# Performance work log

Hardware: AMD Instinct MI355X
Metric: run time of the kernel (lower is better)

## Reference

```python
import jax, jax.numpy as jnp
import numpy as np

PH, PW = 7, 7          # pooled output size
SR = 2                 # sampling_ratio (fixed grid per bin)
SCALE = 0.0625         # spatial_scale = 1/16


def _axis(v, size):
    """Per-axis bilinear setup, faithful to the original clamping logic.
    v: [K] float sample coords. Returns lo, hi int indices, frac l, 1-l, valid mask."""
    valid = (v >= -1.0) & (v <= size)
    vc = jnp.maximum(v, 0.0)
    lo0 = jnp.floor(vc).astype(jnp.int32)
    at_edge = lo0 >= size - 1
    lo = jnp.where(at_edge, size - 1, lo0)
    hi = jnp.where(at_edge, size - 1, lo0 + 1)
    vc = jnp.where(at_edge, jnp.asarray(size - 1, vc.dtype), vc)
    l = vc - lo.astype(vc.dtype)
    return lo, hi, l, 1.0 - l, valid


def roi_align(feat, rois):
    B, C, H, W = feat.shape
    feat_flat = feat.reshape(B, C, H * W)
    grid = (jnp.arange(SR, dtype=feat.dtype) + 0.5) / SR  # sub-bin offsets

    def per_roi(roi):
        b = roi[0].astype(jnp.int32)
        sw, sh = roi[1] * SCALE, roi[2] * SCALE
        ew, eh = roi[3] * SCALE, roi[4] * SCALE
        rw = jnp.maximum(ew - sw, 1.0)
        rh = jnp.maximum(eh - sh, 1.0)
        bh, bw = rh / PH, rw / PW
        # sample coordinates: y[PH,SR], x[PW,SR]
        y = sh + jnp.arange(PH, dtype=feat.dtype)[:, None] * bh + grid[None, :] * bh
        x = sw + jnp.arange(PW, dtype=feat.dtype)[:, None] * bw + grid[None, :] * bw
        y_lo, y_hi, ly, hy, vy = _axis(y.reshape(-1), H)  # [PH*SR]
        x_lo, x_hi, lx, hx, vx = _axis(x.reshape(-1), W)  # [PW*SR]
        valid = (vy[:, None] & vx[None, :]).astype(feat.dtype)  # out-of-range -> zero contribution
        w1 = hy[:, None] * hx[None, :] * valid
        w2 = hy[:, None] * lx[None, :] * valid
        w3 = ly[:, None] * hx[None, :] * valid
        w4 = ly[:, None] * lx[None, :] * valid
        i1 = y_lo[:, None] * W + x_lo[None, :]
        i2 = y_lo[:, None] * W + x_hi[None, :]
        i3 = y_hi[:, None] * W + x_lo[None, :]
        i4 = y_hi[:, None] * W + x_hi[None, :]
        fb = jnp.take(feat_flat, b, axis=0)  # [C, H*W]
        # gather + weighted sum -> [C, PH*SR, PW*SR]
        s = (jnp.take(fb, i1, axis=1) * w1 + jnp.take(fb, i2, axis=1) * w2
             + jnp.take(fb, i3, axis=1) * w3 + jnp.take(fb, i4, axis=1) * w4)
        # average over the SR x SR sampling grid per bin (== / count)
        return s.reshape(C, PH, SR, PW, SR).mean(axis=(2, 4))  # [C, PH, PW]

    return jax.vmap(per_roi)(rois)  # [N, C, PH, PW]


def setup_inputs() -> dict:
    key = jax.random.key(0)
    k1, k2, k3, k4, k5 = jax.random.split(key, 5)
    bottom_data = jax.random.normal(k1, (1, 1024, 50, 50), dtype=jnp.float32)
    n_rois, img = 512, 800.0
    x1 = jax.random.uniform(k2, (n_rois,), minval=0.0, maxval=img - 64.0)
    y1 = jax.random.uniform(k3, (n_rois,), minval=0.0, maxval=img - 64.0)
    bw = jax.random.uniform(k4, (n_rois,), minval=32.0, maxval=256.0)
    bh = jax.random.uniform(k5, (n_rois,), minval=32.0, maxval=256.0)
    x2 = jnp.minimum(x1 + bw, img)
    y2 = jnp.minimum(y1 + bh, img)
    bottom_rois = jnp.stack([jnp.zeros((n_rois,)), x1, y1, x2, y2], axis=1).astype(jnp.float32)
    return {"bottom_data": bottom_data, "bottom_rois": bottom_rois}


def reference(bottom_data, bottom_rois):
    return roi_align(bottom_data, bottom_rois)
```

## Files before the change

kernel.cpp:

```cpp
#include <hip/hip_runtime.h>

#define PH 7
#define PW 7
#define SCALE 0.0625f
#define C_TOTAL 1024
#define H_ 50
#define W_ 50
#define HW_TOTAL (H_ * W_)
#define NROIS 512
#define NBIN (PH * PW)
#define CHB 64
#define NCHUNK (C_TOTAL / CHB)
#define ROWB (W_ * C_TOTAL * 4)
#define COLB (C_TOTAL * 4)
#define RMAX 17
#define GP   65

__global__ __launch_bounds__(256) void transpose_kernel(
    const float* __restrict__ feat, float* __restrict__ featT)
{
    __shared__ float tile[64][65];
    const int hw0 = (blockIdx.x % 40) * 64;
    const int c0  = (blockIdx.x / 40) * 64;
    const int tx = threadIdx.x & 63;
    const int ty = threadIdx.x >> 6;

    const int hw_r = hw0 + tx;
    if (hw_r < HW_TOTAL) {
        #pragma unroll
        for (int j = 0; j < 16; ++j) {
            const int c_l = j * 4 + ty;
            tile[c_l][tx] = feat[(size_t)(c0 + c_l) * HW_TOTAL + hw_r];
        }
    }
    __syncthreads();
    #pragma unroll
    for (int j = 0; j < 16; ++j) {
        const int hw_l = j * 4 + ty;
        const int hw = hw0 + hw_l;
        if (hw < HW_TOTAL)
            featT[(size_t)hw * C_TOTAL + c0 + tx] = tile[tx][hw_l];
    }
}

__device__ __forceinline__ float ldf(const char* base, unsigned byte_off) {
    return *reinterpret_cast<const float*>(base + byte_off);
}

__device__ __forceinline__ float rfl_f(float v) {
    return __uint_as_float(__builtin_amdgcn_readfirstlane(__float_as_uint(v)));
}

__global__ __launch_bounds__(512, 6) void roi_sep_kernel(
    const float* __restrict__ featT,
    const float* __restrict__ rois,
    float* __restrict__ out)
{
    __shared__ __align__(16) float s_G[RMAX * 7 * GP];
    __shared__ __align__(16) int   s_xoff[7][4];
    __shared__ __align__(16) float s_xw[7][4];
    __shared__ __align__(16) int   s_yiT[4][NBIN];
    __shared__ __align__(16) float s_ywT[4][NBIN];

    const int blk    = blockIdx.x;
    const int roi_id = blk >> 4;
    const int chunk  = blk & (NCHUNK - 1);
    const int tid    = threadIdx.x;

    const float* roi = rois + roi_id * 5;

    const float shy = roi[2] * SCALE, ehy = roi[4] * SCALE;
    const float rht = fmaxf(ehy - shy, 1.0f);
    const float bh  = rht * (1.0f / 7.0f);
    int r0 = (int)floorf(fmaxf(shy + 0.25f * bh, 0.0f));
    if (r0 > H_ - 1) r0 = H_ - 1;
    const int lol = (int)floorf(fmaxf(shy + 6.75f * bh, 0.0f));
    int r1 = (lol >= H_ - 1) ? (H_ - 1) : (lol + 1);
    if (r1 - r0 + 1 > RMAX) r1 = r0 + RMAX - 1;
    const int R  = r1 - r0 + 1;

    if (tid < 7) {
        const float swx = roi[1] * SCALE, ewx = roi[3] * SCALE;
        const float rwd = fmaxf(ewx - swx, 1.0f);
        const float bw  = rwd * (1.0f / 7.0f);
        const float base = swx + (float)tid * bw;
        const float v0 = base + 0.25f * bw;
        const float v1 = base + 0.75f * bw;

        int lo0, hi0, lo1, hi1;
        float l0, h0, l1, h1, m0, m1;
        {
            const bool val = (v0 >= -1.0f) && (v0 <= (float)W_);
            float vc = fmaxf(v0, 0.0f);
            int lo = (int)floorf(vc);
            if (lo >= W_ - 1) { lo0 = W_ - 1; hi0 = W_ - 1; vc = (float)(W_ - 1); }
            else              { lo0 = lo; hi0 = lo + 1; }
            l0 = vc - (float)lo0; h0 = 1.0f - l0;
            m0 = val ? 1.0f : 0.0f;
        }
        {
            const bool val = (v1 >= -1.0f) && (v1 <= (float)W_);
            float vc = fmaxf(v1, 0.0f);
            int lo = (int)floorf(vc);
            if (lo >= W_ - 1) { lo1 = W_ - 1; hi1 = W_ - 1; vc = (float)(W_ - 1); }
            else              { lo1 = lo; hi1 = lo + 1; }
            l1 = vc - (float)lo1; h1 = 1.0f - l1;
            m1 = val ? 1.0f : 0.0f;
        }

        float W0 = h0 * m0, W1 = l0 * m0, W2 = h1 * m1, W3 = l1 * m1;
        int I0 = lo0, I1 = hi0, I2 = lo1, I3 = hi1;
        if (I1 == I0) { W0 += W1; W1 = 0.0f; }
        if (I2 == I0) { W0 += W2; W2 = 0.0f; }
        else if (I2 == I1) { W1 += W2; W2 = 0.0f; }
        if (I3 == I0) { W0 += W3; W3 = 0.0f; }
        else if (I3 == I1) { W1 += W3; W3 = 0.0f; }
        else if (I3 == I2) { W2 += W3; W3 = 0.0f; }

        #define CSH(A, B) if (W##A == 0.0f && W##B != 0.0f) { W##A = W##B; I##A = I##B; W##B = 0.0f; }
        CSH(0,1) CSH(1,2) CSH(2,3)
        CSH(0,1) CSH(1,2) CSH(2,3)
        CSH(0,1) CSH(1,2) CSH(2,3)
        #undef CSH

        s_xoff[tid][0] = I0 * COLB; s_xoff[tid][1] = I1 * COLB;
        s_xoff[tid][2] = I2 * COLB; s_xoff[tid][3] = I3 * COLB;
        s_xw[tid][0] = W0; s_xw[tid][1] = W1; s_xw[tid][2] = W2; s_xw[tid][3] = W3;
    }

    if (tid >= 64 && tid < 64 + NBIN) {
        const int bin = tid - 64;
        const int py  = bin / 7, px = bin - py * 7;
        const float base = shy + (float)py * bh;
        const float v0 = base + 0.25f * bh;
        const float v1 = base + 0.75f * bh;

        int lo0, hi0, lo1, hi1;
        float l0, h0, l1, h1, m0, m1;
        {
            const bool val = (v0 >= -1.0f) && (v0 <= (float)H_);
            float vc = fmaxf(v0, 0.0f);
            int lo = (int)floorf(vc);
            if (lo >= H_ - 1) { lo0 = H_ - 1; hi0 = H_ - 1; vc = (float)(H_ - 1); }
            else              { lo0 = lo; hi0 = lo + 1; }
            l0 = vc - (float)lo0; h0 = 1.0f - l0;
            m0 = val ? 0.25f : 0.0f;
        }
        {
            const bool val = (v1 >= -1.0f) && (v1 <= (float)H_);
            float vc = fmaxf(v1, 0.0f);
            int lo = (int)floorf(vc);
            if (lo >= H_ - 1) { lo1 = H_ - 1; hi1 = H_ - 1; vc = (float)(H_ - 1); }
            else              { lo1 = lo; hi1 = lo + 1; }
            l1 = vc - (float)lo1; h1 = 1.0f - l1;
            m1 = val ? 0.25f : 0.0f;
        }

        const int s0 = min(lo0 - r0, RMAX - 1), s1 = min(hi0 - r0, RMAX - 1);
        const int s2 = min(lo1 - r0, RMAX - 1), s3 = min(hi1 - r0, RMAX - 1);
        s_yiT[0][bin] = (s0 * 7 + px) * GP;
        s_yiT[1][bin] = (s1 * 7 + px) * GP;
        s_yiT[2][bin] = (s2 * 7 + px) * GP;
        s_yiT[3][bin] = (s3 * 7 + px) * GP;
        s_ywT[0][bin] = h0 * m0; s_ywT[1][bin] = l0 * m0;
        s_ywT[2][bin] = h1 * m1; s_ywT[3][bin] = l1 * m1;
    }
    __syncthreads();

    int   xo_s[7][4];
    float xw_s[7][4];
    #pragma unroll
    for (int i = 0; i < 7; ++i) {
        const int4   t = *(const int4*)  s_xoff[i];
        const float4 w = *(const float4*)s_xw[i];
        xo_s[i][0] = __builtin_amdgcn_readfirstlane(t.x);
        xo_s[i][1] = __builtin_amdgcn_readfirstlane(t.y);
        xo_s[i][2] = __builtin_amdgcn_readfirstlane(t.z);
        xo_s[i][3] = __builtin_amdgcn_readfirstlane(t.w);
        xw_s[i][0] = rfl_f(w.x); xw_s[i][1] = rfl_f(w.y);
        xw_s[i][2] = rfl_f(w.z); xw_s[i][3] = rfl_f(w.w);
    }

    const int wave = tid >> 6, lane = tid & 63;
    const char* fb  = (const char*)featT;
    const int laneB = (chunk * CHB + lane) * 4;

    for (int rs = wave; rs < R; rs += 8) {
        const unsigned rb = (unsigned)(laneB + (r0 + rs) * ROWB);
        float f[7][4];
        #pragma unroll
        for (int px = 0; px < 7; ++px) {
            f[px][0] = ldf(fb + xo_s[px][0], rb);
            f[px][1] = ldf(fb + xo_s[px][1], rb);
            f[px][2] = ldf(fb + xo_s[px][2], rb);
            f[px][3] = ldf(fb + xo_s[px][3], rb);
        }
        __asm__ __volatile__("" ::: "memory");
        float* gbase = &s_G[rs * 7 * GP + lane];
        #pragma unroll
        for (int px = 0; px < 7; ++px) {
            gbase[px * GP] = (xw_s[px][0] * f[px][0] + xw_s[px][1] * f[px][1])
                           + (xw_s[px][2] * f[px][2] + xw_s[px][3] * f[px][3]);
        }
    }
    __syncthreads();

    float* obase = out + (size_t)roi_id * (C_TOTAL * NBIN)
                       + (size_t)chunk * CHB * NBIN;
    #pragma unroll
    for (int q = 0; q < 3; ++q) {
        const int o   = tid + (q << 9);
        const int c   = o / NBIN;
        const int bin = o - c * NBIN;
        const int i0 = s_yiT[0][bin], i1 = s_yiT[1][bin];
        const int i2 = s_yiT[2][bin], i3 = s_yiT[3][bin];
        const float w0 = s_ywT[0][bin], w1 = s_ywT[1][bin];
        const float w2 = s_ywT[2][bin], w3 = s_ywT[3][bin];
        const float a0 = (w0 * s_G[i0 + c]      + w1 * s_G[i1 + c])
                       + (w2 * s_G[i2 + c]      + w3 * s_G[i3 + c]);
        const float a1 = (w0 * s_G[i0 + c + 32] + w1 * s_G[i1 + c + 32])
                       + (w2 * s_G[i2 + c + 32] + w3 * s_G[i3 + c + 32]);
        __builtin_nontemporal_store(a0, obase + o);
        __builtin_nontemporal_store(a1, obase + o + 1568);
    }
    if (tid < 32) {
        const int o   = tid + 1536;
        const int c   = 31;
        const int bin = o - c * NBIN;
        const int i0 = s_yiT[0][bin], i1 = s_yiT[1][bin];
        const int i2 = s_yiT[2][bin], i3 = s_yiT[3][bin];
        const float w0 = s_ywT[0][bin], w1 = s_ywT[1][bin];
        const float w2 = s_ywT[2][bin], w3 = s_ywT[3][bin];
        const float a0 = (w0 * s_G[i0 + c]      + w1 * s_G[i1 + c])
                       + (w2 * s_G[i2 + c]      + w3 * s_G[i3 + c]);
        const float a1 = (w0 * s_G[i0 + c + 32] + w1 * s_G[i1 + c + 32])
                       + (w2 * s_G[i2 + c + 32] + w3 * s_G[i3 + c + 32]);
        __builtin_nontemporal_store(a0, obase + o);
        __builtin_nontemporal_store(a1, obase + o + 1568);
    }
}

__global__ __launch_bounds__(256) void roi_align_fallback(
    const float* __restrict__ feat,
    const float* __restrict__ rois,
    float* __restrict__ out)
{
    __shared__ float s_w[16][NBIN];
    __shared__ int   s_i[16][NBIN];

    const int blk    = blockIdx.x;
    const int roi_id = blk >> 3;
    const int chunk  = blk & 7;
    const int tid    = threadIdx.x;

    const float* roi = rois + roi_id * 5;

    if (tid < NBIN * 4) {
        const float swx = roi[1] * SCALE;
        const float shy = roi[2] * SCALE;
        const float ewx = roi[3] * SCALE;
        const float ehy = roi[4] * SCALE;
        const float rw = fmaxf(ewx - swx, 1.0f);
        const float rh = fmaxf(ehy - shy, 1.0f);
        const float bw = rw * (1.0f / PW);
        const float bh = rh * (1.0f / PH);

        const int bin = tid >> 2;
        const int s   = tid & 3;
        const int iy  = s >> 1, ix = s & 1;
        const int py  = bin / PW, px = bin % PW;

        const float y = shy + ((float)py + ((float)iy + 0.5f) * 0.5f) * bh;
        const float x = swx + ((float)px + ((float)ix + 0.5f) * 0.5f) * bw;

        const bool vy = (y >= -1.0f) && (y <= (float)H_);
        float yc = fmaxf(y, 0.0f);
        int ylo = (int)floorf(yc);
        int yhi;
        if (ylo >= H_ - 1) { ylo = H_ - 1; yhi = H_ - 1; yc = (float)(H_ - 1); }
        else               { yhi = ylo + 1; }
        const float ly = yc - (float)ylo;
        const float hy = 1.0f - ly;

        const bool vx = (x >= -1.0f) && (x <= (float)W_);
        float xc = fmaxf(x, 0.0f);
        int xlo = (int)floorf(xc);
        int xhi;
        if (xlo >= W_ - 1) { xlo = W_ - 1; xhi = W_ - 1; xc = (float)(W_ - 1); }
        else               { xhi = xlo + 1; }
        const float lx = xc - (float)xlo;
        const float hx = 1.0f - lx;

        const float v = (vy && vx) ? 0.25f : 0.0f;

        const int r = s * 4;
        s_w[r + 0][bin] = hy * hx * v;
        s_w[r + 1][bin] = hy * lx * v;
        s_w[r + 2][bin] = ly * hx * v;
        s_w[r + 3][bin] = ly * lx * v;
        s_i[r + 0][bin] = ylo * W_ + xlo;
        s_i[r + 1][bin] = ylo * W_ + xhi;
        s_i[r + 2][bin] = yhi * W_ + xlo;
        s_i[r + 3][bin] = yhi * W_ + xhi;
    }
    __syncthreads();

    const float* fbase = feat + (size_t)chunk * 128 * HW_TOTAL;
    float* obase = out + (size_t)roi_id * (C_TOTAL * NBIN)
                       + (size_t)chunk * 128 * NBIN;

    for (int o = tid; o < 128 * NBIN; o += 256) {
        const int c   = o / NBIN;
        const int bin = o - c * NBIN;
        const float* f = fbase + c * HW_TOTAL;
        float acc = 0.0f;
        #pragma unroll
        for (int r = 0; r < 16; ++r) acc += s_w[r][bin] * f[s_i[r][bin]];
        obase[o] = acc;
    }
}

extern "C" void kernel_launch(void* const* d_in, const int* in_sizes, int n_in,
                              void* d_out, int out_size, void* d_ws, size_t ws_size,
                              hipStream_t stream) {
    const float* feat = (const float*)d_in[0];
    const float* rois = (const float*)d_in[1];
    float* out = (float*)d_out;

    const size_t need = (size_t)HW_TOTAL * C_TOTAL * sizeof(float);
    if (ws_size >= need) {
        float* featT = (float*)d_ws;
        transpose_kernel<<<dim3(40 * (C_TOTAL / 64)), dim3(256), 0, stream>>>(feat, featT);
        roi_sep_kernel<<<dim3(NROIS * NCHUNK), dim3(512), 0, stream>>>(featT, rois, out);
    } else {
        roi_align_fallback<<<dim3(NROIS * 8), dim3(256), 0, stream>>>(feat, rois, out);
    }
}
```

Before: 54.62 us.

## Precompute per-ROI bilinear tables in the transpose kernel and load them in ROI kernel

The per-ROI x and y sample offsets, weights, r0 and R are now computed once per ROI by the first 512 blocks of the transpose kernel and written to a table after featT in the workspace. The ROI kernel loads these tables from global memory instead of recomputing them in each of its 16 channel-chunk blocks. This removes the redundant setup math and the setup barrier before the gather phase. In exchange it adds global loads of the table, slightly more workspace, and extra work in the transpose kernel.

```diff
diff --git a/kernel.cpp b/kernel.cpp
--- a/kernel.cpp
+++ b/kernel.cpp
@@ -16,8 +16,12 @@
 #define RMAX 17
 #define GP   65
 
+#define TBL_OFF    (HW_TOTAL * C_TOTAL)
+#define TBL_STRIDE 512
+
 __global__ __launch_bounds__(256) void transpose_kernel(
-    const float* __restrict__ feat, float* __restrict__ featT)
+    const float* __restrict__ feat, float* __restrict__ featT,
+    const float* __restrict__ rois)
 {
     __shared__ float tile[64][65];
     const int hw0 = (blockIdx.x % 40) * 64;
@@ -41,33 +45,13 @@
         if (hw < HW_TOTAL)
             featT[(size_t)hw * C_TOTAL + c0 + tx] = tile[tx][hw_l];
     }
-}
-
-__device__ __forceinline__ float ldf(const char* base, unsigned byte_off) {
-    return *reinterpret_cast<const float*>(base + byte_off);
-}
-
-__device__ __forceinline__ float rfl_f(float v) {
-    return __uint_as_float(__builtin_amdgcn_readfirstlane(__float_as_uint(v)));
-}
-
-__global__ __launch_bounds__(512, 6) void roi_sep_kernel(
-    const float* __restrict__ featT,
-    const float* __restrict__ rois,
-    float* __restrict__ out)
-{
-    __shared__ __align__(16) float s_G[RMAX * 7 * GP];
-    __shared__ __align__(16) int   s_xoff[7][4];
-    __shared__ __align__(16) float s_xw[7][4];
-    __shared__ __align__(16) int   s_yiT[4][NBIN];
-    __shared__ __align__(16) float s_ywT[4][NBIN];
-
-    const int blk    = blockIdx.x;
-    const int roi_id = blk >> 4;
-    const int chunk  = blk & (NCHUNK - 1);
-    const int tid    = threadIdx.x;
-
+
+    const int roi_id = blockIdx.x;
+    if (roi_id >= NROIS) return;
     const float* roi = rois + roi_id * 5;
+    float* tbl  = featT + TBL_OFF + (size_t)roi_id * TBL_STRIDE;
+    int*   tbli = (int*)tbl;
+    const int tid = threadIdx.x;
 
     const float shy = roi[2] * SCALE, ehy = roi[4] * SCALE;
     const float rht = fmaxf(ehy - shy, 1.0f);
@@ -78,6 +62,8 @@
     int r1 = (lol >= H_ - 1) ? (H_ - 1) : (lol + 1);
     if (r1 - r0 + 1 > RMAX) r1 = r0 + RMAX - 1;
     const int R  = r1 - r0 + 1;
+
+    if (tid == 128) { tbli[456] = r0; tbli[457] = R; }
 
     if (tid < 7) {
         const float swx = roi[1] * SCALE, ewx = roi[3] * SCALE;
@@ -123,9 +109,10 @@
         CSH(0,1) CSH(1,2) CSH(2,3)
         #undef CSH
 
-        s_xoff[tid][0] = I0 * COLB; s_xoff[tid][1] = I1 * COLB;
-        s_xoff[tid][2] = I2 * COLB; s_xoff[tid][3] = I3 * COLB;
-        s_xw[tid][0] = W0; s_xw[tid][1] = W1; s_xw[tid][2] = W2; s_xw[tid][3] = W3;
+        tbli[tid * 4 + 0] = I0 * COLB; tbli[tid * 4 + 1] = I1 * COLB;
+        tbli[tid * 4 + 2] = I2 * COLB; tbli[tid * 4 + 3] = I3 * COLB;
+        tbl[32 + tid * 4 + 0] = W0; tbl[32 + tid * 4 + 1] = W1;
+        tbl[32 + tid * 4 + 2] = W2; tbl[32 + tid * 4 + 3] = W3;
     }
 
     if (tid >= 64 && tid < 64 + NBIN) {
@@ -158,27 +145,53 @@
 
         const int s0 = min(lo0 - r0, RMAX - 1), s1 = min(hi0 - r0, RMAX - 1);
         const int s2 = min(lo1 - r0, RMAX - 1), s3 = min(hi1 - r0, RMAX - 1);
-        s_yiT[0][bin] = (s0 * 7 + px) * GP;
-        s_yiT[1][bin] = (s1 * 7 + px) * GP;
-        s_yiT[2][bin] = (s2 * 7 + px) * GP;
-        s_yiT[3][bin] = (s3 * 7 + px) * GP;
-        s_ywT[0][bin] = h0 * m0; s_ywT[1][bin] = l0 * m0;
-        s_ywT[2][bin] = h1 * m1; s_ywT[3][bin] = l1 * m1;
-    }
-    __syncthreads();
+        tbli[64 + 0 * NBIN + bin] = (s0 * 7 + px) * GP;
+        tbli[64 + 1 * NBIN + bin] = (s1 * 7 + px) * GP;
+        tbli[64 + 2 * NBIN + bin] = (s2 * 7 + px) * GP;
+        tbli[64 + 3 * NBIN + bin] = (s3 * 7 + px) * GP;
+        tbl[260 + 0 * NBIN + bin] = h0 * m0; tbl[260 + 1 * NBIN + bin] = l0 * m0;
+        tbl[260 + 2 * NBIN + bin] = h1 * m1; tbl[260 + 3 * NBIN + bin] = l1 * m1;
+    }
+}
+
+__device__ __forceinline__ float ldf(const char* base, unsigned byte_off) {
+    return *reinterpret_cast<const float*>(base + byte_off);
+}
+
+__global__ __launch_bounds__(512, 6) void roi_sep_kernel(
+    const float* __restrict__ featT,
+    float* __restrict__ out)
+{
+    __shared__ __align__(16) float s_G[RMAX * 7 * GP];
+    __shared__ __align__(16) float s_ytbl[392];
+
+    const int blk    = blockIdx.x;
+    const int roi_id = blk >> 4;
+    const int chunk  = blk & (NCHUNK - 1);
+    const int tid    = threadIdx.x;
+
+    const float* tbl  = featT + TBL_OFF + (size_t)roi_id * TBL_STRIDE;
+    const int*   tbli = (const int*)tbl;
+
+    if (tid < 392) s_ytbl[tid] = tbl[64 + tid];
+
+    const int r0 = __builtin_amdgcn_readfirstlane(tbli[456]);
+    const int R  = __builtin_amdgcn_readfirstlane(tbli[457]);
 
     int   xo_s[7][4];
     float xw_s[7][4];
     #pragma unroll
     for (int i = 0; i < 7; ++i) {
-        const int4   t = *(const int4*)  s_xoff[i];
-        const float4 w = *(const float4*)s_xw[i];
+        const int4   t = ((const int4*)tbli)[i];
+        const float4 w = ((const float4*)tbl)[8 + i];
         xo_s[i][0] = __builtin_amdgcn_readfirstlane(t.x);
         xo_s[i][1] = __builtin_amdgcn_readfirstlane(t.y);
         xo_s[i][2] = __builtin_amdgcn_readfirstlane(t.z);
         xo_s[i][3] = __builtin_amdgcn_readfirstlane(t.w);
-        xw_s[i][0] = rfl_f(w.x); xw_s[i][1] = rfl_f(w.y);
-        xw_s[i][2] = rfl_f(w.z); xw_s[i][3] = rfl_f(w.w);
+        xw_s[i][0] = __uint_as_float(__builtin_amdgcn_readfirstlane(__float_as_uint(w.x)));
+        xw_s[i][1] = __uint_as_float(__builtin_amdgcn_readfirstlane(__float_as_uint(w.y)));
+        xw_s[i][2] = __uint_as_float(__builtin_amdgcn_readfirstlane(__float_as_uint(w.z)));
+        xw_s[i][3] = __uint_as_float(__builtin_amdgcn_readfirstlane(__float_as_uint(w.w)));
     }
 
     const int wave = tid >> 6, lane = tid & 63;
@@ -205,6 +218,8 @@
     }
     __syncthreads();
 
+    const int* s_yi = (const int*)s_ytbl;
+    const float* s_yw = s_ytbl + 196;
     float* obase = out + (size_t)roi_id * (C_TOTAL * NBIN)
                        + (size_t)chunk * CHB * NBIN;
     #pragma unroll
@@ -212,10 +227,10 @@
         const int o   = tid + (q << 9);
         const int c   = o / NBIN;
         const int bin = o - c * NBIN;
-        const int i0 = s_yiT[0][bin], i1 = s_yiT[1][bin];
-        const int i2 = s_yiT[2][bin], i3 = s_yiT[3][bin];
-        const float w0 = s_ywT[0][bin], w1 = s_ywT[1][bin];
-        const float w2 = s_ywT[2][bin], w3 = s_ywT[3][bin];
+        const int i0 = s_yi[0 * NBIN + bin], i1 = s_yi[1 * NBIN + bin];
+        const int i2 = s_yi[2 * NBIN + bin], i3 = s_yi[3 * NBIN + bin];
+        const float w0 = s_yw[0 * NBIN + bin], w1 = s_yw[1 * NBIN + bin];
+        const float w2 = s_yw[2 * NBIN + bin], w3 = s_yw[3 * NBIN + bin];
         const float a0 = (w0 * s_G[i0 + c]      + w1 * s_G[i1 + c])
                        + (w2 * s_G[i2 + c]      + w3 * s_G[i3 + c]);
         const float a1 = (w0 * s_G[i0 + c + 32] + w1 * s_G[i1 + c + 32])
@@ -227,10 +242,10 @@
         const int o   = tid + 1536;
         const int c   = 31;
         const int bin = o - c * NBIN;
-        const int i0 = s_yiT[0][bin], i1 = s_yiT[1][bin];
-        const int i2 = s_yiT[2][bin], i3 = s_yiT[3][bin];
-        const float w0 = s_ywT[0][bin], w1 = s_ywT[1][bin];
-        const float w2 = s_ywT[2][bin], w3 = s_ywT[3][bin];
+        const int i0 = s_yi[0 * NBIN + bin], i1 = s_yi[1 * NBIN + bin];
+        const int i2 = s_yi[2 * NBIN + bin], i3 = s_yi[3 * NBIN + bin];
+        const float w0 = s_yw[0 * NBIN + bin], w1 = s_yw[1 * NBIN + bin];
+        const float w2 = s_yw[2 * NBIN + bin], w3 = s_yw[3 * NBIN + bin];
         const float a0 = (w0 * s_G[i0 + c]      + w1 * s_G[i1 + c])
                        + (w2 * s_G[i2 + c]      + w3 * s_G[i3 + c]);
         const float a1 = (w0 * s_G[i0 + c + 32] + w1 * s_G[i1 + c + 32])
@@ -327,11 +342,11 @@
     const float* rois = (const float*)d_in[1];
     float* out = (float*)d_out;
 
-    const size_t need = (size_t)HW_TOTAL * C_TOTAL * sizeof(float);
+    const size_t need = (size_t)(TBL_OFF + NROIS * TBL_STRIDE) * sizeof(float);
     if (ws_size >= need) {
         float* featT = (float*)d_ws;
-        transpose_kernel<<<dim3(40 * (C_TOTAL / 64)), dim3(256), 0, stream>>>(feat, featT);
-        roi_sep_kernel<<<dim3(NROIS * NCHUNK), dim3(512), 0, stream>>>(featT, rois, out);
+        transpose_kernel<<<dim3(40 * (C_TOTAL / 64)), dim3(256), 0, stream>>>(feat, featT, rois);
+        roi_sep_kernel<<<dim3(NROIS * NCHUNK), dim3(512), 0, stream>>>(featT, out);
     } else {
         roi_align_fallback<<<dim3(NROIS * 8), dim3(256), 0, stream>>>(feat, rois, out);
     }
```

After: 48.34 us (median of 2 runs). 1.13x faster.
